# Performance work log

Measured on AMD Instinct MI355X. Metric: run time of the kernel, lower is better.

## Reference

```python
import jax, jax.numpy as jnp
import numpy as np

B, N, D, E = 8, 2048, 2048, 64
CAP = 64


def setup_inputs() -> dict:
    key = jax.random.key(0)
    k1, k2 = jax.random.split(key)
    token_inputs = jax.random.normal(k1, (B, N, D), dtype=jnp.float32)
    w_gate = jax.random.normal(k2, (D, E), dtype=jnp.float32)
    return {"token_inputs": token_inputs, "w_gate": w_gate, "expert_capacity": CAP}


def reference(token_inputs, w_gate, expert_capacity):
    # gate projection: [b,n,d] x [d,e] -> [b,n,e]
    router_logits = jnp.einsum('bnd,de->bne', token_inputs, w_gate)
    # router z-loss: mean over tokens of logsumexp(logits)^2
    z = jax.nn.logsumexp(router_logits, axis=-1)
    router_z_loss = jnp.mean(z * z)
    router_probs = jax.nn.softmax(router_logits, axis=-1)
    num_experts = router_probs.shape[-1]
    # top-1 expert per token (Switch routing)
    expert_gate = jnp.max(router_probs, axis=-1)           # [b,n]
    expert_index = jnp.argmax(router_probs, axis=-1)       # [b,n]
    expert_mask = jax.nn.one_hot(expert_index, num_experts, dtype=router_probs.dtype)  # [b,n,e]
    # position of each token within its chosen expert's buffer (0-based);
    # -1 where the token did not pick that expert
    position_in_expert = jnp.cumsum(expert_mask, axis=1) * expert_mask - 1.0  # [b,n,e]
    # one_hot zeroes out positions < 0 or >= capacity (capacity overflow drop)
    dispatch_mask = jax.nn.one_hot(position_in_expert.astype(jnp.int32),
                                   expert_capacity, dtype=router_probs.dtype)  # [b,n,e,c]
    combine_array = dispatch_mask * expert_gate[..., None, None]               # [b,n,e,c]
    return dispatch_mask, combine_array, router_z_loss
```

## Files before the change

### kernel.cpp

```cpp
#include <hip/hip_runtime.h>
#include <cstdint>
#include <cstddef>

#define B_ 8
#define N_ 2048
#define D_ 2048
#define E_ 64
#define CAP_ 64
#define NTOK (B_*N_)
#define GEMM_BLOCKS 256
#define FILL_BLOCKS 3584
#define DC 64
#define NTILE (D_/DC)
#define MASK_ELEMS ((size_t)NTOK*(size_t)E_*(size_t)CAP_)

typedef float f32x4 __attribute__((ext_vector_type(4)));
typedef short bf16x8 __attribute__((ext_vector_type(8)));
typedef unsigned int u32;
typedef u32 u32x2 __attribute__((ext_vector_type(2)));

__device__ __forceinline__ u32 f2bf(float f) {
  u32 u = __float_as_uint(f);
  return (u + 0x7fffu + ((u >> 16) & 1u)) >> 16;
}
__device__ __forceinline__ float bf2f(u32 b) { return __uint_as_float(b << 16); }

__global__ __launch_bounds__(256)
void k_wconv(const float* __restrict__ W, u32* __restrict__ whi, u32* __restrict__ wlo) {
  const int i = blockIdx.x * 256 + threadIdx.x;
  const int g = i & 7, e = (i >> 3) & 63, t = i >> 9;
  const int d0 = t * DC + g * 8;
  const int dst = ((t * 64 + e) * 8 + (g ^ (e & 7))) * 4;
  #pragma unroll
  for (int jj = 0; jj < 4; ++jj) {
    const float x0 = W[(size_t)(d0 + 2*jj    ) * E_ + e];
    const float x1 = W[(size_t)(d0 + 2*jj + 1) * E_ + e];
    const u32 h0 = f2bf(x0), h1 = f2bf(x1);
    const u32 l0 = f2bf(x0 - bf2f(h0)), l1 = f2bf(x1 - bf2f(h1));
    whi[dst + jj] = h0 | (h1 << 16);
    wlo[dst + jj] = l0 | (l1 << 16);
  }
}

__global__ __launch_bounds__(256)
void k_gemm_zero(const float* __restrict__ X, const u32* __restrict__ whi,
                 const u32* __restrict__ wlo, float* __restrict__ out,
                 float* __restrict__ gate_ws, int* __restrict__ idx_ws,
                 float* __restrict__ z_ws) {
  const int bid = blockIdx.x;
  if (bid >= GEMM_BLOCKS) {
    const int zb = bid - GEMM_BLOCKS;
    f32x4* o4 = (f32x4*)out;
    const size_t total4 = (2*MASK_ELEMS) / 4;
    const size_t stride = (size_t)FILL_BLOCKS * 256;
    const f32x4 z4 = {0.f, 0.f, 0.f, 0.f};
    for (size_t i = (size_t)zb*256 + threadIdx.x; i < total4; i += stride)
      __builtin_nontemporal_store(z4, &o4[i]);
    if (zb == 0 && threadIdx.x == 0) out[2*MASK_ELEMS] = 0.f;
    return;
  }

  __shared__ __align__(16) char lds[2][32768];
  const int tid  = threadIdx.x;
  const int lane = tid & 63;
  const int wid  = __builtin_amdgcn_readfirstlane(tid >> 6);
  const int tokbase = bid * 64;
  const int woff = wid * 16;
  const int rA = lane & 15, kg = lane >> 4;

  int xr_r[4], xr_q[4], xw_off[4];
  #pragma unroll
  for (int p = 0; p < 4; ++p) {
    const int c = p*256 + tid;
    const int r = c >> 4, q = c & 15;
    xr_r[p] = r; xr_q[p] = q;
    xw_off[p] = r*128 + (((q >> 1) ^ (r & 7)) << 4) + ((q & 1) << 3);
  }
  const f32x4* xg   = (const f32x4*)X;
  const f32x4* whi4 = (const f32x4*)whi;
  const f32x4* wlo4 = (const f32x4*)wlo;

  f32x4 xr[4], wr[4];

#define XW_LOAD(t)                                                            \
  { _Pragma("unroll")                                                         \
    for (int p = 0; p < 4; ++p)                                               \
      xr[p] = xg[(size_t)(tokbase + xr_r[p])*512 + (size_t)(t)*16 + xr_q[p]]; \
    wr[0] = whi4[(size_t)(t)*512 + tid];                                      \
    wr[1] = whi4[(size_t)(t)*512 + 256 + tid];                                \
    wr[2] = wlo4[(size_t)(t)*512 + tid];                                      \
    wr[3] = wlo4[(size_t)(t)*512 + 256 + tid]; }

#define XW_STORE(buf)                                                         \
  { char* bq = lds[buf];                                                      \
    _Pragma("unroll")                                                         \
    for (int p = 0; p < 4; ++p) {                                             \
      const u32 h0 = f2bf(xr[p][0]), h1 = f2bf(xr[p][1]);                     \
      const u32 h2 = f2bf(xr[p][2]), h3 = f2bf(xr[p][3]);                     \
      const u32 l0 = f2bf(xr[p][0] - bf2f(h0)), l1 = f2bf(xr[p][1] - bf2f(h1)); \
      const u32 l2 = f2bf(xr[p][2] - bf2f(h2)), l3 = f2bf(xr[p][3] - bf2f(h3)); \
      u32x2 hp; hp[0] = h0 | (h1 << 16); hp[1] = h2 | (h3 << 16);             \
      u32x2 lp; lp[0] = l0 | (l1 << 16); lp[1] = l2 | (l3 << 16);             \
      *(u32x2*)(bq + xw_off[p])        = hp;                                  \
      *(u32x2*)(bq + 8192 + xw_off[p]) = lp;                                  \
    }                                                                         \
    *(f32x4*)(bq + 16384 +        tid*16) = wr[0];                            \
    *(f32x4*)(bq + 16384 + 4096 + tid*16) = wr[1];                            \
    *(f32x4*)(bq + 24576 +        tid*16) = wr[2];                            \
    *(f32x4*)(bq + 24576 + 4096 + tid*16) = wr[3]; }

  XW_LOAD(0);
  XW_STORE(0);
  __syncthreads();

  f32x4 acc[4];
  #pragma unroll
  for (int eb = 0; eb < 4; ++eb) { acc[eb][0]=0.f; acc[eb][1]=0.f; acc[eb][2]=0.f; acc[eb][3]=0.f; }

  const int tokrow = woff + rA;
  for (int t = 0; t < NTILE; ++t) {
    if (t + 1 < NTILE) XW_LOAD(t + 1);

    const char* bp = lds[t & 1];
    #pragma unroll
    for (int kk = 0; kk < 2; ++kk) {
      const int gA = ((kk*4 + kg) ^ (rA & 7)) << 4;
      const bf16x8 Ah = *(const bf16x8*)(bp +        tokrow*128 + gA);
      const bf16x8 Al = *(const bf16x8*)(bp + 8192 + tokrow*128 + gA);
      #pragma unroll
      for (int eb = 0; eb < 4; ++eb) {
        const int e  = eb*16 + rA;
        const int gB = ((kk*4 + kg) ^ (e & 7)) << 4;
        const bf16x8 Bh = *(const bf16x8*)(bp + 16384 + e*128 + gB);
        const bf16x8 Bl = *(const bf16x8*)(bp + 24576 + e*128 + gB);
        acc[eb] = __builtin_amdgcn_mfma_f32_16x16x32_bf16(Ah, Bh, acc[eb], 0, 0, 0);
        acc[eb] = __builtin_amdgcn_mfma_f32_16x16x32_bf16(Ah, Bl, acc[eb], 0, 0, 0);
        acc[eb] = __builtin_amdgcn_mfma_f32_16x16x32_bf16(Al, Bh, acc[eb], 0, 0, 0);
        acc[eb] = __builtin_amdgcn_mfma_f32_16x16x32_bf16(Al, Bl, acc[eb], 0, 0, 0);
      }
    }

    if (t + 1 < NTILE) XW_STORE((t + 1) & 1);
    __syncthreads();
  }

  float* Lg = (float*)&lds[0][0];
  #pragma unroll
  for (int eb = 0; eb < 4; ++eb)
    #pragma unroll
    for (int r = 0; r < 4; ++r)
      Lg[(woff + kg*4 + r)*65 + eb*16 + rA] = acc[eb][r];
  __syncthreads();

  #pragma unroll 1
  for (int i = 0; i < 16; ++i) {
    const int tkn = woff + i;
    const float v = Lg[tkn*65 + lane];
    float vmax = v; int vidx = lane;
    #pragma unroll
    for (int m = 1; m < 64; m <<= 1) {
      const float om = __shfl_xor(vmax, m);
      const int   oi = __shfl_xor(vidx, m);
      if (om > vmax || (om == vmax && oi < vidx)) { vmax = om; vidx = oi; }
    }
    float se = expf(v - vmax);
    #pragma unroll
    for (int m = 1; m < 64; m <<= 1) se += __shfl_xor(se, m);
    if (lane == 0) {
      const int row = tokbase + tkn;
      gate_ws[row] = 1.0f / se;
      idx_ws[row]  = vidx;
      z_ws[row]    = vmax + logf(se);
    }
  }
#undef XW_LOAD
#undef XW_STORE
}

__global__ __launch_bounds__(64)
void k_route(const float* __restrict__ gate_ws, const int* __restrict__ idx_ws,
             const float* __restrict__ z_ws, float* __restrict__ out) {
  const int b    = blockIdx.x;
  const int lane = threadIdx.x;
  float* dispatch = out;
  float* combine  = out + MASK_ELEMS;

  int   cnt  = 0;
  float zsum = 0.f;
  const unsigned long long below = (1ULL << lane) - 1ULL;

  for (int n0 = 0; n0 < N_; n0 += 64) {
    const int   t    = b*N_ + n0 + lane;
    const int   idx  = idx_ws[t];
    const float gate = gate_ws[t];
    const float z    = z_ws[t];
    zsum += z * z;

    unsigned long long bb[6];
    #pragma unroll
    for (int k = 0; k < 6; ++k) bb[k] = __ballot((idx >> k) & 1);

    unsigned long long m_tok = ~0ULL, m_exp = ~0ULL;
    #pragma unroll
    for (int k = 0; k < 6; ++k) {
      m_tok &= ((idx  >> k) & 1) ? bb[k] : ~bb[k];
      m_exp &= ((lane >> k) & 1) ? bb[k] : ~bb[k];
    }

    const int rank = __popcll(m_tok & below);
    const int base = __shfl(cnt, idx);
    const int pos  = base + rank;
    cnt += __popcll(m_exp);

    if (pos < CAP_) {
      const size_t o = (((size_t)t)*E_ + (size_t)idx)*CAP_ + (size_t)pos;
      dispatch[o] = 1.0f;
      combine[o]  = gate;
    }
  }

  #pragma unroll
  for (int m = 1; m < 64; m <<= 1) zsum += __shfl_xor(zsum, m);
  if (lane == 0) atomicAdd(out + 2*MASK_ELEMS, zsum * (1.0f / (float)NTOK));
}

extern "C" void kernel_launch(void* const* d_in, const int* in_sizes, int n_in,
                              void* d_out, int out_size, void* d_ws, size_t ws_size,
                              hipStream_t stream) {
  const float* X = (const float*)d_in[0];
  const float* W = (const float*)d_in[1];
  float* out = (float*)d_out;

  char* wsb = (char*)d_ws;
  u32*   whi     = (u32*)  (wsb);
  u32*   wlo     = (u32*)  (wsb + 262144);
  float* gate_ws = (float*)(wsb + 524288);
  int*   idx_ws  = (int*)  (wsb + 589824);
  float* z_ws    = (float*)(wsb + 655360);

  hipLaunchKernelGGL(k_wconv, dim3(64), dim3(256), 0, stream, W, whi, wlo);
  hipLaunchKernelGGL(k_gemm_zero, dim3(GEMM_BLOCKS + FILL_BLOCKS), dim3(256), 0, stream,
                     X, whi, wlo, out, gate_ws, idx_ws, z_ws);
  hipLaunchKernelGGL(k_route, dim3(B_), dim3(64), 0, stream,
                     gate_ws, idx_ws, z_ws, out);
}
```

Baseline: 140.7 us.

## Move mask zero-fill after routing and write values in a single fill pass

The output zero-fill no longer runs inside the GEMM launch. The router kernel now emits a compact per-token code holding the expert and its slot. A new fill kernel then writes the complete dispatch and combine arrays, zeros and nonzeros together, in one streaming pass, and also stores the z-loss. This drops the scattered second writes and the atomic, and the GEMM runs without contention from the fill. In exchange the fill can no longer overlap the GEMM, and routing now runs as a single block that serialises the per-batch scans.

Result: slower. 178.7 us (+27.0%).

```diff
diff --git a/kernel.cpp b/kernel.cpp
--- a/kernel.cpp
+++ b/kernel.cpp
@@ -9,7 +9,7 @@
 #define CAP_ 64
 #define NTOK (B_*N_)
 #define GEMM_BLOCKS 256
-#define FILL_BLOCKS 3584
+#define FILLV_BLOCKS 2048
 #define DC 64
 #define NTILE (D_/DC)
 #define MASK_ELEMS ((size_t)NTOK*(size_t)E_*(size_t)CAP_)
@@ -43,22 +43,10 @@
 }
 
 __global__ __launch_bounds__(256)
-void k_gemm_zero(const float* __restrict__ X, const u32* __restrict__ whi,
-                 const u32* __restrict__ wlo, float* __restrict__ out,
-                 float* __restrict__ gate_ws, int* __restrict__ idx_ws,
-                 float* __restrict__ z_ws) {
+void k_gemm(const float* __restrict__ X, const u32* __restrict__ whi,
+            const u32* __restrict__ wlo, float* __restrict__ gate_ws,
+            int* __restrict__ idx_ws, float* __restrict__ z_ws) {
   const int bid = blockIdx.x;
-  if (bid >= GEMM_BLOCKS) {
-    const int zb = bid - GEMM_BLOCKS;
-    f32x4* o4 = (f32x4*)out;
-    const size_t total4 = (2*MASK_ELEMS) / 4;
-    const size_t stride = (size_t)FILL_BLOCKS * 256;
-    const f32x4 z4 = {0.f, 0.f, 0.f, 0.f};
-    for (size_t i = (size_t)zb*256 + threadIdx.x; i < total4; i += stride)
-      __builtin_nontemporal_store(z4, &o4[i]);
-    if (zb == 0 && threadIdx.x == 0) out[2*MASK_ELEMS] = 0.f;
-    return;
-  }
 
   __shared__ __align__(16) char lds[2][32768];
   const int tid  = threadIdx.x;
@@ -177,13 +165,13 @@
 #undef XW_STORE
 }
 
-__global__ __launch_bounds__(64)
+__global__ __launch_bounds__(512)
 void k_route(const float* __restrict__ gate_ws, const int* __restrict__ idx_ws,
-             const float* __restrict__ z_ws, float* __restrict__ out) {
-  const int b    = blockIdx.x;
-  const int lane = threadIdx.x;
-  float* dispatch = out;
-  float* combine  = out + MASK_ELEMS;
+             const float* __restrict__ z_ws, u32* __restrict__ code_ws,
+             float* __restrict__ zacc) {
+  __shared__ float zpart[8];
+  const int lane = threadIdx.x & 63;
+  const int b    = threadIdx.x >> 6;
 
   int   cnt  = 0;
   float zsum = 0.f;
@@ -192,7 +180,6 @@
   for (int n0 = 0; n0 < N_; n0 += 64) {
     const int   t    = b*N_ + n0 + lane;
     const int   idx  = idx_ws[t];
-    const float gate = gate_ws[t];
     const float z    = z_ws[t];
     zsum += z * z;
 
@@ -212,16 +199,49 @@
     const int pos  = base + rank;
     cnt += __popcll(m_exp);
 
-    if (pos < CAP_) {
-      const size_t o = (((size_t)t)*E_ + (size_t)idx)*CAP_ + (size_t)pos;
-      dispatch[o] = 1.0f;
-      combine[o]  = gate;
-    }
+    code_ws[t] = (u32)idx | ((u32)((pos < CAP_) ? pos : 255) << 8);
   }
 
   #pragma unroll
   for (int m = 1; m < 64; m <<= 1) zsum += __shfl_xor(zsum, m);
-  if (lane == 0) atomicAdd(out + 2*MASK_ELEMS, zsum * (1.0f / (float)NTOK));
+  if (lane == 0) zpart[b] = zsum;
+  __syncthreads();
+  if (threadIdx.x == 0) {
+    float s = 0.f;
+    #pragma unroll
+    for (int i = 0; i < 8; ++i) s += zpart[i];
+    zacc[0] = s * (1.0f / (float)NTOK);
+  }
+}
+
+__global__ __launch_bounds__(256)
+void k_fillv(const u32* __restrict__ code_ws, const float* __restrict__ gate_ws,
+             const float* __restrict__ zacc, float* __restrict__ out) {
+  const size_t g0     = (size_t)blockIdx.x * 256 + threadIdx.x;
+  const size_t ngran  = MASK_ELEMS / 4;
+  const size_t stride = (size_t)FILLV_BLOCKS * 256;
+  f32x4* disp = (f32x4*)out;
+  f32x4* comb = (f32x4*)(out + MASK_ELEMS);
+
+  for (size_t g = g0; g < ngran; g += stride) {
+    const int t  = (int)(g >> 10);
+    const u32 r  = (u32)g & 1023u;
+    const int e  = (int)(r >> 4);
+    const int c0 = (int)(r & 15u) << 2;
+    const u32 code = code_ws[t];
+    f32x4 dv = {0.f, 0.f, 0.f, 0.f};
+    f32x4 cv = {0.f, 0.f, 0.f, 0.f};
+    if (e == (int)(code & 0xFFu)) {
+      const int p = (int)(code >> 8) - c0;
+      if (0 <= p && p < 4) {
+        dv[p] = 1.0f;
+        cv[p] = gate_ws[t];
+      }
+    }
+    __builtin_nontemporal_store(dv, disp + g);
+    __builtin_nontemporal_store(cv, comb + g);
+  }
+  if (g0 == 0) out[2*MASK_ELEMS] = zacc[0];
 }
 
 extern "C" void kernel_launch(void* const* d_in, const int* in_sizes, int n_in,
@@ -237,10 +257,14 @@
   float* gate_ws = (float*)(wsb + 524288);
   int*   idx_ws  = (int*)  (wsb + 589824);
   float* z_ws    = (float*)(wsb + 655360);
+  u32*   code_ws = (u32*)  (wsb + 720896);
+  float* zacc    = (float*)(wsb + 786432);
 
   hipLaunchKernelGGL(k_wconv, dim3(64), dim3(256), 0, stream, W, whi, wlo);
-  hipLaunchKernelGGL(k_gemm_zero, dim3(GEMM_BLOCKS + FILL_BLOCKS), dim3(256), 0, stream,
-                     X, whi, wlo, out, gate_ws, idx_ws, z_ws);
-  hipLaunchKernelGGL(k_route, dim3(B_), dim3(64), 0, stream,
-                     gate_ws, idx_ws, z_ws, out);
-}
+  hipLaunchKernelGGL(k_gemm, dim3(GEMM_BLOCKS), dim3(256), 0, stream,
+                     X, whi, wlo, gate_ws, idx_ws, z_ws);
+  hipLaunchKernelGGL(k_route, dim3(1), dim3(512), 0, stream,
+                     gate_ws, idx_ws, z_ws, code_ws, zacc);
+  hipLaunchKernelGGL(k_fillv, dim3(FILLV_BLOCKS), dim3(256), 0, stream,
+                     code_ws, gate_ws, zacc, out);
+}
```
